# Kernel tuning notes

Hardware: AMD Instinct MI355X
Metric: run time of the kernel (lower is better)

## Reference

```python
import jax, jax.numpy as jnp
import numpy as np

NQ, NT, D = 2048, 131072, 64   # query nodes, target nodes, feature dim
E = 2_000_000                  # candidate (u, v) edges
M = 1024                       # consensus (nn_map) pairs; vc = top M rows of Xt


def setup_inputs() -> dict:
    key = jax.random.key(0)
    ks = jax.random.split(key, 8)
    Xq = jax.random.normal(ks[0], (NQ, D), dtype=jnp.float32)
    Xt = jax.random.normal(ks[1], (NT, D), dtype=jnp.float32)
    W_alpha = jax.random.normal(ks[2], (D, D), dtype=jnp.float32) * 0.05
    b_alpha = jax.random.normal(ks[3], (1,), dtype=jnp.float32) * 0.05
    W_beta = jax.random.normal(ks[4], (D, D), dtype=jnp.float32) * 0.05
    b_beta = jax.random.normal(ks[5], (1,), dtype=jnp.float32) * 0.05
    u_idx = jax.random.randint(ks[6], (E,), 0, NQ, dtype=jnp.int32)
    # candidate targets live in [0, NT - M); consensus targets in [NT - M, NT)
    v_idx = jax.random.randint(ks[7], (E,), 0, NT - M, dtype=jnp.int32)
    uc = jax.random.randint(jax.random.fold_in(key, 7), (M,), 0, NQ, dtype=jnp.int32)
    vc = (NT - M) + jnp.arange(M, dtype=jnp.int32)
    return {"Xq": Xq, "Xt": Xt, "W_alpha": W_alpha, "b_alpha": b_alpha,
            "W_beta": W_beta, "b_beta": b_beta,
            "u_idx": u_idx, "v_idx": v_idx, "uc": uc, "vc": vc}


def reference(Xq, Xt, W_alpha, b_alpha, W_beta, b_beta, u_idx, v_idx, uc, vc):
    # 1) consensus overwrite: Xt[vc] = Xq[uc]  (nn_map)
    Xt_c = Xt.at[vc].set(Xq[uc])

    # 2) per-edge gather + bilinear interaction scoring
    xq_e = Xq[u_idx]      # [E, D]
    xt_e = Xt_c[v_idx]    # [E, D]

    def bilinear(W, b):
        return jnp.einsum('ed,df,ef->e', xq_e, W, xt_e) + b[0]

    beta = jax.nn.sigmoid(bilinear(W_beta, b_beta))   # [E] gate
    alpha = jax.nn.elu(bilinear(W_alpha, b_alpha))    # [E] score
    h_e = (1.0 - beta)[:, None] * xq_e + beta[:, None] * xt_e  # [E, D]

    # 3) segment softmax over incoming u per target v (== masked softmax over Nq)
    m = jax.ops.segment_max(alpha, v_idx, num_segments=NT)     # -inf on empty segments
    a = jnp.exp(alpha - m[v_idx])
    s = jax.ops.segment_sum(a, v_idx, num_segments=NT)
    a = a / s[v_idx] + 1e-10   # matches original +1e-10 after normalization

    # 4) scatter-aggregate weighted messages back into Xt rows with >=1 candidate
    agg = jax.ops.segment_sum(a[:, None] * h_e, v_idx, num_segments=NT)  # [NT, D]
    deg = jax.ops.segment_sum(jnp.ones_like(alpha), v_idx, num_segments=NT)
    Xt_out = jnp.where((deg > 0)[:, None], agg, Xt_c)
    return (Xq, Xt_out)
```

## Files before the change

kernel.cpp:

```cpp
#include <hip/hip_runtime.h>

#define NQ 2048
#define NT 131072
#define DD 64
#define MM 1024
#define NBUCK 512
#define BCAP 4608
#define CHUNK 4096


typedef __attribute__((ext_vector_type(2))) _Float16 h2;

#if defined(__has_builtin)
#if __has_builtin(__builtin_amdgcn_fdot2)
#define HAVE_FDOT2 1
#endif
#endif

__device__ __forceinline__ float fdot2(h2 a, h2 b, float c) {
#ifdef HAVE_FDOT2
    return __builtin_amdgcn_fdot2(a, b, c, false);
#else
    return fmaf((float)a.x, (float)b.x, fmaf((float)a.y, (float)b.y, c));
#endif
}

__global__ void yq_kernel(const float* __restrict__ Xq,
                          const float* __restrict__ Wa,
                          const float* __restrict__ Wb,
                          _Float16* __restrict__ Yab16,
                          _Float16* __restrict__ Xq16) {
    int r = blockIdx.x * 4 + (threadIdx.x >> 6);
    int j = threadIdx.x & 63;
    float sa = 0.f, sb = 0.f;
#pragma unroll
    for (int k = 0; k < DD; ++k) {
        float x = Xq[r * DD + k];
        sa = fmaf(x, Wa[k * DD + j], sa);
        sb = fmaf(x, Wb[k * DD + j], sb);
    }
    int gbase = r * 128 + (j >> 2) * 8 + (j & 3);
    Yab16[gbase] = (_Float16)sa;
    Yab16[gbase + 4] = (_Float16)sb;
    Xq16[r * DD + j] = (_Float16)Xq[r * DD + j];
}

__global__ __launch_bounds__(1024) void bin_kernel(
        const int* __restrict__ u_idx, const int* __restrict__ v_idx,
        int* __restrict__ gcur, unsigned* __restrict__ gbuf, int E) {
    __shared__ unsigned stage[CHUNK];
    __shared__ int hist[NBUCK], off[NBUCK], base[NBUCK], cur[NBUCK];
    int tid = threadIdx.x;
    int e0 = blockIdx.x * CHUNK;
    int n = min(CHUNK, E - e0);
    if (n <= 0) return;

    for (int i = tid; i < NBUCK; i += 1024) hist[i] = 0;
    __syncthreads();

    unsigned p[4];
    int nv = 0;
    int i0 = tid * 4;
    if (i0 + 3 < n) {
        int4 u4 = *(const int4*)(u_idx + e0 + i0);
        int4 v4 = *(const int4*)(v_idx + e0 + i0);
        p[0] = ((unsigned)v4.x << 11) | (unsigned)u4.x;
        p[1] = ((unsigned)v4.y << 11) | (unsigned)u4.y;
        p[2] = ((unsigned)v4.z << 11) | (unsigned)u4.z;
        p[3] = ((unsigned)v4.w << 11) | (unsigned)u4.w;
        nv = 4;
    } else {
        for (int j = 0; j < 4; ++j) {
            if (i0 + j < n) {
                p[j] = ((unsigned)v_idx[e0 + i0 + j] << 11) | (unsigned)u_idx[e0 + i0 + j];
                ++nv;
            }
        }
    }
    for (int j = 0; j < nv; ++j) atomicAdd(&hist[p[j] >> 19], 1);
    __syncthreads();
    if (tid < 64) {
        int h[8], sum = 0;
#pragma unroll
        for (int j = 0; j < 8; ++j) { h[j] = hist[8 * tid + j]; sum += h[j]; }
        int incl = sum;
#pragma unroll
        for (int d = 1; d < 64; d <<= 1) {
            int y = __shfl_up(incl, d, 64);
            if (tid >= d) incl += y;
        }
        int excl = incl - sum;
#pragma unroll
        for (int j = 0; j < 8; ++j) { off[8 * tid + j] = excl; excl += h[j]; }
    }
    __syncthreads();
    for (int i = tid; i < NBUCK; i += 1024) {
        base[i] = hist[i] ? atomicAdd(&gcur[i], hist[i]) : 0;
        cur[i] = off[i];
    }
    __syncthreads();
    for (int j = 0; j < nv; ++j) {
        int pos = atomicAdd(&cur[p[j] >> 19], 1);
        stage[pos] = p[j];
    }
    __syncthreads();
    for (int i = tid; i < n; i += 1024) {
        unsigned q = stage[i];
        int b = q >> 19;
        int idx = base[b] + (i - off[b]);
        if (idx < BCAP) gbuf[(size_t)b * BCAP + idx] = q;
    }
}

template <int CTRL>
__device__ __forceinline__ float dpp_add(float x) {
    int xi = __builtin_bit_cast(int, x);
    int yi = __builtin_amdgcn_update_dpp(xi, xi, CTRL, 0xF, 0xF, true);
    return x + __builtin_bit_cast(float, yi);
}
__device__ __forceinline__ float red16(float x) {
    x = dpp_add<0xB1>(x);
    x = dpp_add<0x4E>(x);
    x = dpp_add<0x124>(x);
    x = dpp_add<0x128>(x);
    return x;
}

__global__ __launch_bounds__(1024, 2) void bucket_kernel(
        const float* __restrict__ Xq,
        const float* __restrict__ Xt,
        const _Float16* __restrict__ Yab16,
        const _Float16* __restrict__ Xq16,
        const float* __restrict__ ba,
        const float* __restrict__ bb,
        const int* __restrict__ gcur,
        const unsigned* __restrict__ gbuf,
        const int* __restrict__ uc,
        float* __restrict__ outXt) {
    __shared__ unsigned short su[BCAP];
    __shared__ int hist[256], cur[256], rstart[257];
    int tid = threadIdx.x;
    int b = blockIdx.x;
    int n = min(gcur[b], BCAP);

    if (tid < 256) hist[tid] = 0;
    __syncthreads();
    for (int i = tid; i < n; i += 1024)
        atomicAdd(&hist[(gbuf[(size_t)b * BCAP + i] >> 11) & 255], 1);
    __syncthreads();
    if (tid < 64) {
        int h0 = hist[4 * tid], h1 = hist[4 * tid + 1];
        int h2_ = hist[4 * tid + 2], h3 = hist[4 * tid + 3];
        int tot = h0 + h1 + h2_ + h3;
        int incl = tot;
#pragma unroll
        for (int d = 1; d < 64; d <<= 1) {
            int y = __shfl_up(incl, d, 64);
            if (tid >= d) incl += y;
        }
        int excl = incl - tot;
        rstart[4 * tid] = excl;             cur[4 * tid] = excl;
        rstart[4 * tid + 1] = excl + h0;    cur[4 * tid + 1] = excl + h0;
        rstart[4 * tid + 2] = excl + h0 + h1;       cur[4 * tid + 2] = excl + h0 + h1;
        rstart[4 * tid + 3] = excl + h0 + h1 + h2_; cur[4 * tid + 3] = excl + h0 + h1 + h2_;
        if (tid == 63) rstart[256] = excl + tot;
    }
    __syncthreads();
    for (int i = tid; i < n; i += 1024) {
        unsigned p = gbuf[(size_t)b * BCAP + i];
        int pos = atomicAdd(&cur[(p >> 11) & 255], 1);
        su[pos] = (unsigned short)(p & 0x7FFu);
    }
    __syncthreads();

    int lane = tid & 63;
    int w = tid >> 6;
    int l16 = lane & 15;
    int g = lane >> 4;
    float ba0 = ba[0], bb0 = bb[0];

    for (int r = w; r < 256; r += 16) {
        int v = (b << 8) + r;
        int startr = rstart[r];
        int deg = rstart[r + 1] - startr;
        if (deg == 0) {
            if (g == 0) {
                float4 o;
                if (v >= NT - MM) {
                    int u = uc[v - (NT - MM)];
                    o = ((const float4*)(Xq + (size_t)u * DD))[l16];
                } else {
                    o = ((const float4*)(Xt + (size_t)v * DD))[l16];
                }
                ((float4*)(outXt + (size_t)v * DD))[l16] = o;
            }
            continue;
        }
        float4 xt4 = ((const float4*)(Xt + (size_t)v * DD))[l16];
        h2 xt01, xt23;
        xt01.x = (_Float16)xt4.x; xt01.y = (_Float16)xt4.y;
        xt23.x = (_Float16)xt4.z; xt23.y = (_Float16)xt4.w;
        float4 acc = make_float4(0.f, 0.f, 0.f, 0.f);
        float s = 0.f;
        for (int base = 0; base < deg; base += 8) {
            int e0 = base + g;
            int e1 = base + 4 + g;
            bool ok0 = e0 < deg, ok1 = e1 < deg;
            int u0 = (int)su[startr + (ok0 ? e0 : 0)];
            int u1 = (int)su[startr + (ok1 ? e1 : 0)];
            float4 y0 = ((const float4*)(Yab16 + (u0 << 7)))[l16];
            float4 y1 = ((const float4*)(Yab16 + (u1 << 7)))[l16];
            float2 xv0 = ((const float2*)(Xq16 + (u0 << 6)))[l16];
            float2 xv1 = ((const float2*)(Xq16 + (u1 << 6)))[l16];
            float pa0 = fdot2(__builtin_bit_cast(h2, y0.y), xt23,
                       fdot2(__builtin_bit_cast(h2, y0.x), xt01, 0.f));
            float pb0 = fdot2(__builtin_bit_cast(h2, y0.w), xt23,
                       fdot2(__builtin_bit_cast(h2, y0.z), xt01, 0.f));
            float pa1 = fdot2(__builtin_bit_cast(h2, y1.y), xt23,
                       fdot2(__builtin_bit_cast(h2, y1.x), xt01, 0.f));
            float pb1 = fdot2(__builtin_bit_cast(h2, y1.w), xt23,
                       fdot2(__builtin_bit_cast(h2, y1.z), xt01, 0.f));
            pa0 = red16(pa0); pb0 = red16(pb0);
            pa1 = red16(pa1); pb1 = red16(pb1);
            float la0 = pa0 + ba0, la1 = pa1 + ba0;
            float t0 = __expf(la0), t1 = __expf(la1);
            float al0 = la0 > 0.f ? la0 : (t0 - 1.f);
            float al1 = la1 > 0.f ? la1 : (t1 - 1.f);
            float a0 = ok0 ? __expf(al0) : 0.f;
            float a1 = ok1 ? __expf(al1) : 0.f;
            float be0 = __builtin_amdgcn_rcpf(1.f + __expf(-(pb0 + bb0)));
            float be1 = __builtin_amdgcn_rcpf(1.f + __expf(-(pb1 + bb0)));
            h2 q0a = __builtin_bit_cast(h2, xv0.x), q0b = __builtin_bit_cast(h2, xv0.y);
            h2 q1a = __builtin_bit_cast(h2, xv1.x), q1b = __builtin_bit_cast(h2, xv1.y);
            float x0x = (float)q0a.x, x0y = (float)q0a.y, x0z = (float)q0b.x, x0w = (float)q0b.y;
            float x1x = (float)q1a.x, x1y = (float)q1a.y, x1z = (float)q1b.x, x1w = (float)q1b.y;
            float4 h0v, h1v;
            h0v.x = fmaf(be0, xt4.x - x0x, x0x);
            h0v.y = fmaf(be0, xt4.y - x0y, x0y);
            h0v.z = fmaf(be0, xt4.z - x0z, x0z);
            h0v.w = fmaf(be0, xt4.w - x0w, x0w);
            h1v.x = fmaf(be1, xt4.x - x1x, x1x);
            h1v.y = fmaf(be1, xt4.y - x1y, x1y);
            h1v.z = fmaf(be1, xt4.z - x1z, x1z);
            h1v.w = fmaf(be1, xt4.w - x1w, x1w);
            acc.x = fmaf(a0, h0v.x, fmaf(a1, h1v.x, acc.x));
            acc.y = fmaf(a0, h0v.y, fmaf(a1, h1v.y, acc.y));
            acc.z = fmaf(a0, h0v.z, fmaf(a1, h1v.z, acc.z));
            acc.w = fmaf(a0, h0v.w, fmaf(a1, h1v.w, acc.w));
            s += a0 + a1;
        }
        acc.x += __shfl_xor(acc.x, 16, 64);
        acc.y += __shfl_xor(acc.y, 16, 64);
        acc.z += __shfl_xor(acc.z, 16, 64);
        acc.w += __shfl_xor(acc.w, 16, 64);
        s     += __shfl_xor(s, 16, 64);
        acc.x += __shfl_xor(acc.x, 32, 64);
        acc.y += __shfl_xor(acc.y, 32, 64);
        acc.z += __shfl_xor(acc.z, 32, 64);
        acc.w += __shfl_xor(acc.w, 32, 64);
        s     += __shfl_xor(s, 32, 64);
        if (g == 0) {
            float inv = __builtin_amdgcn_rcpf(s);
            float4 o = make_float4(acc.x * inv, acc.y * inv, acc.z * inv, acc.w * inv);
            ((float4*)(outXt + (size_t)v * DD))[l16] = o;
        }
    }
}

extern "C" void kernel_launch(void* const* d_in, const int* in_sizes, int n_in,
                              void* d_out, int out_size, void* d_ws, size_t ws_size,
                              hipStream_t stream) {
    const float* Xq = (const float*)d_in[0];
    const float* Xt = (const float*)d_in[1];
    const float* Wa = (const float*)d_in[2];
    const float* ba = (const float*)d_in[3];
    const float* Wb = (const float*)d_in[4];
    const float* bb = (const float*)d_in[5];
    const int* u_idx = (const int*)d_in[6];
    const int* v_idx = (const int*)d_in[7];
    const int* uc = (const int*)d_in[8];
    const int* vc = (const int*)d_in[9];
    const int E = in_sizes[6];
    (void)vc;

    float* out = (float*)d_out;
    float* outXq = out;
    float* outXt = out + NQ * DD;

    char* ws = (char*)d_ws;
    _Float16* Yab16 = (_Float16*)ws;  ws += (size_t)NQ * 2 * DD * sizeof(_Float16);
    _Float16* Xq16 = (_Float16*)ws;   ws += (size_t)NQ * DD * sizeof(_Float16);
    int* gcur = (int*)ws;             ws += NBUCK * sizeof(int);
    ws = (char*)(((size_t)ws + 255) & ~(size_t)255);
    unsigned* gbuf = (unsigned*)ws;   ws += (size_t)NBUCK * BCAP * sizeof(unsigned);

    hipMemcpyAsync(outXq, Xq, NQ * DD * sizeof(float), hipMemcpyDeviceToDevice, stream);
    hipMemsetAsync(gcur, 0, NBUCK * sizeof(int), stream);

    yq_kernel<<<NQ / 4, 256, 0, stream>>>(Xq, Wa, Wb, Yab16, Xq16);

    int nchunks = (E + CHUNK - 1) / CHUNK;
    bin_kernel<<<nchunks, 1024, 0, stream>>>(u_idx, v_idx, gcur, gbuf, E);

    bucket_kernel<<<NBUCK, 1024, 0, stream>>>(Xq, Xt, Yab16, Xq16, ba, bb, gcur, gbuf,
                                              uc, outXt);
}
```

Baseline: 207.2 us.

## Fuse projection and Xq copy into bin kernel; factor xt term out of edge loop

Merges the Xq projection kernel and the Xq output memcpy into the binning kernel as extra blocks, which removes one launch and one copy. In the bucket kernel the per-edge message blend is rewritten algebraically: the xt contribution is gathered into a scalar sum of a*beta and applied once per target row, so the inner loop does fewer FMAs per edge. The cost is an extra scalar accumulator and shuffle reduction, plus slightly different floating-point rounding.

```diff
diff --git a/kernel.cpp b/kernel.cpp
--- a/kernel.cpp
+++ b/kernel.cpp
@@ -25,32 +25,37 @@
 #endif
 }
 
-__global__ void yq_kernel(const float* __restrict__ Xq,
-                          const float* __restrict__ Wa,
-                          const float* __restrict__ Wb,
-                          _Float16* __restrict__ Yab16,
-                          _Float16* __restrict__ Xq16) {
-    int r = blockIdx.x * 4 + (threadIdx.x >> 6);
-    int j = threadIdx.x & 63;
-    float sa = 0.f, sb = 0.f;
-#pragma unroll
-    for (int k = 0; k < DD; ++k) {
-        float x = Xq[r * DD + k];
-        sa = fmaf(x, Wa[k * DD + j], sa);
-        sb = fmaf(x, Wb[k * DD + j], sb);
-    }
-    int gbase = r * 128 + (j >> 2) * 8 + (j & 3);
-    Yab16[gbase] = (_Float16)sa;
-    Yab16[gbase + 4] = (_Float16)sb;
-    Xq16[r * DD + j] = (_Float16)Xq[r * DD + j];
-}
-
-__global__ __launch_bounds__(1024) void bin_kernel(
+__global__ __launch_bounds__(1024) void bin_yq_kernel(
         const int* __restrict__ u_idx, const int* __restrict__ v_idx,
-        int* __restrict__ gcur, unsigned* __restrict__ gbuf, int E) {
+        int* __restrict__ gcur, unsigned* __restrict__ gbuf,
+        const float* __restrict__ Xq,
+        const float* __restrict__ Wa, const float* __restrict__ Wb,
+        _Float16* __restrict__ Yab16, _Float16* __restrict__ Xq16,
+        float* __restrict__ outXq, int E) {
     __shared__ unsigned stage[CHUNK];
     __shared__ int hist[NBUCK], off[NBUCK], base[NBUCK], cur[NBUCK];
     int tid = threadIdx.x;
+    int nchunks = (E + CHUNK - 1) / CHUNK;
+
+    if (blockIdx.x >= nchunks) {
+        int r = (blockIdx.x - nchunks) * 16 + (tid >> 6);
+        int j = tid & 63;
+        float sa = 0.f, sb = 0.f;
+#pragma unroll
+        for (int k = 0; k < DD; ++k) {
+            float x = Xq[r * DD + k];
+            sa = fmaf(x, Wa[k * DD + j], sa);
+            sb = fmaf(x, Wb[k * DD + j], sb);
+        }
+        int gbase = r * 128 + (j >> 2) * 8 + (j & 3);
+        Yab16[gbase] = (_Float16)sa;
+        Yab16[gbase + 4] = (_Float16)sb;
+        float xj = Xq[r * DD + j];
+        Xq16[r * DD + j] = (_Float16)xj;
+        outXq[r * DD + j] = xj;
+        return;
+    }
+
     int e0 = blockIdx.x * CHUNK;
     int n = min(CHUNK, E - e0);
     if (n <= 0) return;
@@ -202,6 +207,7 @@
         xt23.x = (_Float16)xt4.z; xt23.y = (_Float16)xt4.w;
         float4 acc = make_float4(0.f, 0.f, 0.f, 0.f);
         float s = 0.f;
+        float s2 = 0.f;
         for (int base = 0; base < deg; base += 8) {
             int e0 = base + g;
             int e1 = base + 4 + g;
@@ -230,38 +236,40 @@
             float a1 = ok1 ? __expf(al1) : 0.f;
             float be0 = __builtin_amdgcn_rcpf(1.f + __expf(-(pb0 + bb0)));
             float be1 = __builtin_amdgcn_rcpf(1.f + __expf(-(pb1 + bb0)));
+            float c20 = a0 * be0, c21 = a1 * be1;
+            float c10 = a0 - c20, c11 = a1 - c21;
             h2 q0a = __builtin_bit_cast(h2, xv0.x), q0b = __builtin_bit_cast(h2, xv0.y);
             h2 q1a = __builtin_bit_cast(h2, xv1.x), q1b = __builtin_bit_cast(h2, xv1.y);
-            float x0x = (float)q0a.x, x0y = (float)q0a.y, x0z = (float)q0b.x, x0w = (float)q0b.y;
-            float x1x = (float)q1a.x, x1y = (float)q1a.y, x1z = (float)q1b.x, x1w = (float)q1b.y;
-            float4 h0v, h1v;
-            h0v.x = fmaf(be0, xt4.x - x0x, x0x);
-            h0v.y = fmaf(be0, xt4.y - x0y, x0y);
-            h0v.z = fmaf(be0, xt4.z - x0z, x0z);
-            h0v.w = fmaf(be0, xt4.w - x0w, x0w);
-            h1v.x = fmaf(be1, xt4.x - x1x, x1x);
-            h1v.y = fmaf(be1, xt4.y - x1y, x1y);
-            h1v.z = fmaf(be1, xt4.z - x1z, x1z);
-            h1v.w = fmaf(be1, xt4.w - x1w, x1w);
-            acc.x = fmaf(a0, h0v.x, fmaf(a1, h1v.x, acc.x));
-            acc.y = fmaf(a0, h0v.y, fmaf(a1, h1v.y, acc.y));
-            acc.z = fmaf(a0, h0v.z, fmaf(a1, h1v.z, acc.z));
-            acc.w = fmaf(a0, h0v.w, fmaf(a1, h1v.w, acc.w));
+            acc.x = fmaf((float)q0a.x, c10, acc.x);
+            acc.y = fmaf((float)q0a.y, c10, acc.y);
+            acc.z = fmaf((float)q0b.x, c10, acc.z);
+            acc.w = fmaf((float)q0b.y, c10, acc.w);
+            acc.x = fmaf((float)q1a.x, c11, acc.x);
+            acc.y = fmaf((float)q1a.y, c11, acc.y);
+            acc.z = fmaf((float)q1b.x, c11, acc.z);
+            acc.w = fmaf((float)q1b.y, c11, acc.w);
             s += a0 + a1;
+            s2 += c20 + c21;
         }
         acc.x += __shfl_xor(acc.x, 16, 64);
         acc.y += __shfl_xor(acc.y, 16, 64);
         acc.z += __shfl_xor(acc.z, 16, 64);
         acc.w += __shfl_xor(acc.w, 16, 64);
         s     += __shfl_xor(s, 16, 64);
+        s2    += __shfl_xor(s2, 16, 64);
         acc.x += __shfl_xor(acc.x, 32, 64);
         acc.y += __shfl_xor(acc.y, 32, 64);
         acc.z += __shfl_xor(acc.z, 32, 64);
         acc.w += __shfl_xor(acc.w, 32, 64);
         s     += __shfl_xor(s, 32, 64);
+        s2    += __shfl_xor(s2, 32, 64);
         if (g == 0) {
             float inv = __builtin_amdgcn_rcpf(s);
-            float4 o = make_float4(acc.x * inv, acc.y * inv, acc.z * inv, acc.w * inv);
+            float4 o;
+            o.x = fmaf(s2, xt4.x, acc.x) * inv;
+            o.y = fmaf(s2, xt4.y, acc.y) * inv;
+            o.z = fmaf(s2, xt4.z, acc.z) * inv;
+            o.w = fmaf(s2, xt4.w, acc.w) * inv;
             ((float4*)(outXt + (size_t)v * DD))[l16] = o;
         }
     }
@@ -294,13 +302,11 @@
     ws = (char*)(((size_t)ws + 255) & ~(size_t)255);
     unsigned* gbuf = (unsigned*)ws;   ws += (size_t)NBUCK * BCAP * sizeof(unsigned);
 
-    hipMemcpyAsync(outXq, Xq, NQ * DD * sizeof(float), hipMemcpyDeviceToDevice, stream);
     hipMemsetAsync(gcur, 0, NBUCK * sizeof(int), stream);
 
-    yq_kernel<<<NQ / 4, 256, 0, stream>>>(Xq, Wa, Wb, Yab16, Xq16);
-
     int nchunks = (E + CHUNK - 1) / CHUNK;
-    bin_kernel<<<nchunks, 1024, 0, stream>>>(u_idx, v_idx, gcur, gbuf, E);
+    bin_yq_kernel<<<nchunks + NQ / 16, 1024, 0, stream>>>(
+        u_idx, v_idx, gcur, gbuf, Xq, Wa, Wb, Yab16, Xq16, outXq, E);
 
     bucket_kernel<<<NBUCK, 1024, 0, stream>>>(Xq, Xt, Yab16, Xq16, ba, bb, gcur, gbuf,
                                               uc, outXt);
```

New measurement: 205.8 us. Within noise of the previous version (-0.7%).
